# Optimization experiments

Hardware: AMD Instinct MI355X
Metric: run time of the kernel (lower is better)

The kernel has to match this reference:

```python
import jax, jax.numpy as jnp
import numpy as np

N_NODES = 40962
N_EDGES = 245760
K = 10  # gaussian kernels
D = 2   # pseudo-coordinate dim
EPS = 1e-15


def gmm_conv(x, edge_index, pseudo, g, mu, sigma, root, bias):
    """PyG GMMConv with aggr='mean', root_weight=True.
    x: [N, Cin], edge_index: [2, E] (row 0 = source j, row 1 = target i),
    pseudo: [E, D], g: [Cin, K*Cout], mu/sigma: [K, D], root: [Cin, Cout], bias: [Cout].
    """
    src, dst = edge_index[0], edge_index[1]
    E = pseudo.shape[0]
    # Gaussian mixture edge weights: [E, K]
    diff = pseudo[:, None, :] - mu[None, :, :]                     # [E, K, D]
    w = jnp.exp(jnp.sum(-0.5 * diff * diff / (EPS + sigma[None] ** 2), axis=-1))
    xj = x[src]                                                    # [E, Cin] gather
    y = (xj @ g).reshape(E, K, -1)                                 # [E, K, Cout]
    msg = jnp.sum(y * w[:, :, None], axis=1)                       # [E, Cout]
    agg = jax.ops.segment_sum(msg, dst, num_segments=N_NODES)      # scatter-add
    deg = jax.ops.segment_sum(jnp.ones((E,), x.dtype), dst, num_segments=N_NODES)
    agg = agg / jnp.maximum(deg, 1.0)[:, None]                     # mean aggregation
    return agg + x @ root + bias


def setup_inputs() -> dict:
    key = jax.random.key(0)
    ks = jax.random.split(key, 20)
    Cin, Ch, Cout = 64, 64, 128
    sc = lambda fan: 1.0 / np.sqrt(fan)
    inp = {
        "x": jax.random.normal(ks[0], (N_NODES, Cin), jnp.float32),
        "edge_index": jax.random.randint(ks[1], (2, N_EDGES), 0, N_NODES, jnp.int32),
        "pseudo": jax.random.uniform(ks[2], (N_EDGES, D), jnp.float32),
        # conv1: Cin -> Ch
        "g1": jax.random.normal(ks[3], (Cin, K * Ch), jnp.float32) * sc(Cin),
        "mu1": jax.random.uniform(ks[4], (K, D), jnp.float32),
        "sigma1": jax.random.uniform(ks[5], (K, D), jnp.float32) + 0.5,
        "root1": jax.random.normal(ks[6], (Cin, Ch), jnp.float32) * sc(Cin),
        "b1": jnp.zeros((Ch,), jnp.float32),
        # conv2: Ch -> Cout
        "g2": jax.random.normal(ks[7], (Ch, K * Cout), jnp.float32) * sc(Ch),
        "mu2": jax.random.uniform(ks[8], (K, D), jnp.float32),
        "sigma2": jax.random.uniform(ks[9], (K, D), jnp.float32) + 0.5,
        "root2": jax.random.normal(ks[10], (Ch, Cout), jnp.float32) * sc(Ch),
        "b2": jnp.zeros((Cout,), jnp.float32),
        # shortcut: Cin -> Cout (size_in != size_out)
        "gs": jax.random.normal(ks[11], (Cin, K * Cout), jnp.float32) * sc(Cin),
        "mus": jax.random.uniform(ks[12], (K, D), jnp.float32),
        "sigmas": jax.random.uniform(ks[13], (K, D), jnp.float32) + 0.5,
        "roots": jax.random.normal(ks[14], (Cin, Cout), jnp.float32) * sc(Cin),
        "bs": jnp.zeros((Cout,), jnp.float32),
    }
    return inp


def reference(x, edge_index, pseudo, g1, mu1, sigma1, root1, b1,
              g2, mu2, sigma2, root2, b2, gs, mus, sigmas, roots, bs):
    h = gmm_conv(x, edge_index, pseudo, g1, mu1, sigma1, root1, b1)
    h = jax.nn.relu(h)
    y = gmm_conv(h, edge_index, pseudo, g2, mu2, sigma2, root2, b2)
    x_s = gmm_conv(x, edge_index, pseudo, gs, mus, sigmas, roots, bs)
    return jax.nn.relu(y + x_s)
```

## Files before the change

kernel.cpp:

```cpp
#include <hip/hip_runtime.h>
#include <hip/hip_bf16.h>

using bf16 = __hip_bfloat16;
typedef __attribute__((ext_vector_type(8))) short short8;
typedef __attribute__((ext_vector_type(4))) float float4v;

#define N_NODES 40962
#define N_EDGES 245760
#define NP      41024
#define KG      10
#define SCAN_B  256
#define NBLK    ((NP + SCAN_B - 1) / SCAN_B)
#define GRIDF   (NP / 16)

#define CVT_V   (N_NODES * 64 / 8)
#define CVT_BLK ((CVT_V + 255) / 256)
#define W3_BLK  (N_EDGES / 256)
#define PACK_N  (64 * 704 + 2 * 128 * 704)
#define PACK_BLK (PACK_N / 256)

#define ZRS  680
#define ZT   10880

__device__ __forceinline__ float ldf(const void* p, size_t i, int isf32) {
    return isf32 ? ((const float*)p)[i] : __bfloat162float(((const bf16*)p)[i]);
}
__device__ __forceinline__ float blo(unsigned u) { return __uint_as_float(u << 16); }
__device__ __forceinline__ float bhi(unsigned u) { return __uint_as_float(u & 0xffff0000u); }
__device__ __forceinline__ unsigned pk2(float a, float b) {
    union { bf16 h[2]; unsigned u; } t;
    t.h[0] = __float2bfloat16(a);
    t.h[1] = __float2bfloat16(b);
    return t.u;
}
__device__ __forceinline__ int rfl(int v) { return __builtin_amdgcn_readfirstlane(v); }

__global__ void k_detect_count(const void* x, const int* __restrict__ ei,
                               int* __restrict__ flag, int* __restrict__ deg) {
    if (blockIdx.x == 0) {
        __shared__ int huge_c, zero_even;
        if (threadIdx.x == 0) { huge_c = 0; zero_even = 0; }
        __syncthreads();
        const bf16* xb = (const bf16*)x;
        int lh = 0, lz = 0;
        for (int i = threadIdx.x; i < 8192; i += 256) {
            float v = __bfloat162float(xb[i]);
            if (!(fabsf(v) <= 1e4f)) lh++;
            if ((i & 1) == 0 && v == 0.0f) lz++;
        }
        atomicAdd(&huge_c, lh);
        atomicAdd(&zero_even, lz);
        __syncthreads();
        if (threadIdx.x == 0) flag[0] = (huge_c > 0 || zero_even > 3000) ? 1 : 0;
    } else {
        int e = (blockIdx.x - 1) * 256 + threadIdx.x;
        if (e < N_EDGES) atomicAdd(&deg[ei[N_EDGES + e]], 1);
    }
}

__global__ void k_scan1(const int* __restrict__ deg, int* __restrict__ offs,
                        int* __restrict__ bsum) {
    __shared__ int buf[SCAN_B];
    int t = threadIdx.x, b = blockIdx.x;
    int i = b * SCAN_B + t;
    int v = (i < NP) ? deg[i] : 0;
    buf[t] = v;
    __syncthreads();
    for (int off = 1; off < SCAN_B; off <<= 1) {
        int a = (t >= off) ? buf[t - off] : 0;
        __syncthreads();
        buf[t] += a;
        __syncthreads();
    }
    if (i < NP) offs[i] = buf[t] - v;
    if (t == SCAN_B - 1) bsum[b] = buf[t];
}

__global__ void k_scan3m(int* __restrict__ offs, const int* __restrict__ bsum,
                         const int* __restrict__ deg, int* __restrict__ cur,
                         float* __restrict__ invdeg) {
    __shared__ int buf[256];
    int t = threadIdx.x, b = blockIdx.x;
    int v = (t < NBLK) ? bsum[t] : 0;
    buf[t] = v;
    __syncthreads();
    for (int off = 1; off < 256; off <<= 1) {
        int a = (t >= off) ? buf[t - off] : 0;
        __syncthreads();
        buf[t] += a;
        __syncthreads();
    }
    int bofs = (b > 0) ? buf[b - 1] : 0;
    int total = buf[NBLK - 1];
    int i = b * 256 + t;
    if (i < NP) {
        int o = offs[i] + bofs;
        offs[i] = o;
        cur[i] = o;
        int d = deg[i];
        invdeg[i] = 1.0f / (float)(d > 1 ? d : 1);
    }
    if (i == 0) offs[NP] = total;
}

__global__ void k_fill(const int* __restrict__ ei, int* __restrict__ cur,
                       int* __restrict__ ep, int* __restrict__ csr_src) {
    int e = blockIdx.x * 256 + threadIdx.x;
    if (e < N_EDGES) {
        int pos = atomicAdd(&cur[ei[N_EDGES + e]], 1);
        ep[e] = pos;
        csr_src[pos] = ei[e];
    }
}

__device__ __forceinline__ void gw_one(float p0, float p1, const void* mu,
                                       const void* sg, int f, float* out) {
#pragma unroll
    for (int k = 0; k < KG; k++) {
        float m0 = ldf(mu, 2 * k + 0, f), m1 = ldf(mu, 2 * k + 1, f);
        float s0 = ldf(sg, 2 * k + 0, f), s1 = ldf(sg, 2 * k + 1, f);
        float d0 = p0 - m0, d1 = p1 - m1;
        float t = -0.5f * (d0 * d0 / (1e-15f + s0 * s0) + d1 * d1 / (1e-15f + s1 * s1));
        out[k] = __expf(t);
    }
}

__device__ __forceinline__ void pack_frag(const void* g, const void* root, int f,
                                          int idx, int Cout, bf16* Bp) {
    int j = idx & 7;
    int lane = (idx >> 3) & 63;
    int rem = idx >> 9;
    int kc = rem % 22;
    int n = rem / 22;
    int col = n * 16 + (lane & 15);
    int k = kc * 32 + (lane >> 4) * 8 + j;
    float v;
    if (k < 512) {
        int cin = k >> 3, kg = k & 7;
        v = ldf(g, (size_t)cin * (KG * Cout) + (size_t)kg * Cout + col, f);
    } else if (k < 640) {
        int jj = k - 512;
        int cin = jj >> 1, kg = 8 + (jj & 1);
        v = ldf(g, (size_t)cin * (KG * Cout) + (size_t)kg * Cout + col, f);
    } else {
        v = ldf(root, (size_t)(k - 640) * Cout + col, f);
    }
    Bp[idx] = __float2bfloat16(v);
}

__global__ void k_prep_all(const void* __restrict__ x, const void* __restrict__ pseudo,
                           const void* mu1, const void* sg1, const void* mu2,
                           const void* sg2, const void* mus, const void* sgs,
                           const void* g1, const void* root1, const void* g2,
                           const void* root2, const void* gs, const void* roots,
                           const int* __restrict__ flag, const int* __restrict__ ep,
                           bf16* __restrict__ Xf, unsigned* __restrict__ wcab,
                           unsigned* __restrict__ wc2, bf16* wt1p, bf16* wt2p,
                           bf16* wtsp) {
    int b = blockIdx.x;
    int tid = threadIdx.x;
    int f = flag[0];
    if (b < CVT_BLK) {
        int i = b * 256 + tid;
        if (i < CVT_V) {
            int node = i >> 3, j = i & 7;
            uint4 u;
            if (f) {
                const float4* xf = (const float4*)x;
                float4 a = xf[2 * i], c = xf[2 * i + 1];
                union { bf16 t[8]; uint4 u; } tt;
                tt.t[0] = __float2bfloat16(a.x); tt.t[1] = __float2bfloat16(a.y);
                tt.t[2] = __float2bfloat16(a.z); tt.t[3] = __float2bfloat16(a.w);
                tt.t[4] = __float2bfloat16(c.x); tt.t[5] = __float2bfloat16(c.y);
                tt.t[6] = __float2bfloat16(c.z); tt.t[7] = __float2bfloat16(c.w);
                u = tt.u;
            } else {
                u = ((const uint4*)x)[i];
            }
            *(uint4*)(Xf + (size_t)node * 64 + j * 8) = u;
        }
    } else if (b < CVT_BLK + W3_BLK) {
        int e = (b - CVT_BLK) * 256 + tid;
        float p0 = ldf(pseudo, (size_t)e * 2 + 0, f);
        float p1 = ldf(pseudo, (size_t)e * 2 + 1, f);
        float o1[KG], o2[KG], os[KG];
        gw_one(p0, p1, mu1, sg1, f, o1);
        gw_one(p0, p1, mu2, sg2, f, o2);
        gw_one(p0, p1, mus, sgs, f, os);
        int pos = ep[e];
        unsigned* d = wcab + (size_t)pos * 10;
        d[0] = pk2(o1[0], o1[1]); d[1] = pk2(o1[2], o1[3]);
        d[2] = pk2(o1[4], o1[5]); d[3] = pk2(o1[6], o1[7]);
        d[4] = pk2(o1[8], o1[9]);
        d[5] = pk2(os[0], os[1]); d[6] = pk2(os[2], os[3]);
        d[7] = pk2(os[4], os[5]); d[8] = pk2(os[6], os[7]);
        d[9] = pk2(os[8], os[9]);
        unsigned* d2 = wc2 + (size_t)pos * 5;
        d2[0] = pk2(o2[0], o2[1]); d2[1] = pk2(o2[2], o2[3]);
        d2[2] = pk2(o2[4], o2[5]); d2[3] = pk2(o2[6], o2[7]);
        d2[4] = pk2(o2[8], o2[9]);
    } else {
        int idx = (b - CVT_BLK - W3_BLK) * 256 + tid;
        if (idx < 64 * 704) {
            pack_frag(g1, root1, f, idx, 64, wt1p);
        } else if (idx < 64 * 704 + 128 * 704) {
            pack_frag(g2, root2, f, idx - 64 * 704, 128, wt2p);
        } else {
            pack_frag(gs, roots, f, idx - 64 * 704 - 128 * 704, 128, wtsp);
        }
    }
}

__device__ __forceinline__ float ldxf(const bf16* X, int src, int lane) {
    return __bfloat162float(X[(size_t)src * 64 + lane]);
}

__device__ __forceinline__ int clampe(int idx) {
    return idx > N_EDGES - 1 ? N_EDGES - 1 : idx;
}

__device__ __forceinline__ void store_zlds(bf16* z, int r, int lane, const float* a,
                                           float inv) {
    union { bf16 h[8]; uint4 u; } p;
#pragma unroll
    for (int k = 0; k < 8; k++) p.h[k] = __float2bfloat16(a[k] * inv);
    *(uint4*)(z + r * ZRS + lane * 8) = p.u;
    *(unsigned*)(z + r * ZRS + 512 + lane * 2) = pk2(a[8] * inv, a[9] * inv);
}

__device__ __forceinline__ void gather_dual(const int* __restrict__ offs,
                                            const int* __restrict__ csr_src,
                                            const unsigned* __restrict__ wb,
                                            const bf16* __restrict__ X, int node,
                                            int lane, float* aa, float* ab) {
#pragma unroll
    for (int k = 0; k < KG; k++) { aa[k] = 0.0f; ab[k] = 0.0f; }
    int beg = rfl(offs[node]);
    int end = rfl(offs[node + 1]);
    int cnt = end - beg;
    int s4 = rfl(csr_src[clampe(beg + 4)]);
    float xv0 = ldxf(X, rfl(csr_src[clampe(beg + 0)]), lane);
    float xv1 = ldxf(X, rfl(csr_src[clampe(beg + 1)]), lane);
    float xv2 = ldxf(X, rfl(csr_src[clampe(beg + 2)]), lane);
    float xv3 = ldxf(X, rfl(csr_src[clampe(beg + 3)]), lane);
    const unsigned* wp0 = wb + (size_t)clampe(beg + 0) * 10;
    unsigned c0 = wp0[0], c1 = wp0[1], c2 = wp0[2], c3 = wp0[3], c4 = wp0[4];
    unsigned c5 = wp0[5], c6 = wp0[6], c7 = wp0[7], c8 = wp0[8], c9 = wp0[9];
    const unsigned* wp1 = wb + (size_t)clampe(beg + 1) * 10;
    unsigned n0 = wp1[0], n1 = wp1[1], n2 = wp1[2], n3 = wp1[3], n4 = wp1[4];
    unsigned n5 = wp1[5], n6 = wp1[6], n7 = wp1[7], n8 = wp1[8], n9 = wp1[9];
    for (int t = 0; t < cnt; ++t) {
        int s5 = rfl(csr_src[clampe(beg + t + 5)]);
        float xv4 = ldxf(X, s4, lane);
        const unsigned* wp2 = wb + (size_t)clampe(beg + t + 2) * 10;
        unsigned m0 = wp2[0], m1 = wp2[1], m2 = wp2[2], m3 = wp2[3], m4 = wp2[4];
        unsigned m5 = wp2[5], m6 = wp2[6], m7 = wp2[7], m8 = wp2[8], m9 = wp2[9];
        aa[0] += blo(c0) * xv0; aa[1] += bhi(c0) * xv0;
        aa[2] += blo(c1) * xv0; aa[3] += bhi(c1) * xv0;
        aa[4] += blo(c2) * xv0; aa[5] += bhi(c2) * xv0;
        aa[6] += blo(c3) * xv0; aa[7] += bhi(c3) * xv0;
        aa[8] += blo(c4) * xv0; aa[9] += bhi(c4) * xv0;
        ab[0] += blo(c5) * xv0; ab[1] += bhi(c5) * xv0;
        ab[2] += blo(c6) * xv0; ab[3] += bhi(c6) * xv0;
        ab[4] += blo(c7) * xv0; ab[5] += bhi(c7) * xv0;
        ab[6] += blo(c8) * xv0; ab[7] += bhi(c8) * xv0;
        ab[8] += blo(c9) * xv0; ab[9] += bhi(c9) * xv0;
        xv0 = xv1; xv1 = xv2; xv2 = xv3; xv3 = xv4; s4 = s5;
        c0 = n0; c1 = n1; c2 = n2; c3 = n3; c4 = n4;
        c5 = n5; c6 = n6; c7 = n7; c8 = n8; c9 = n9;
        n0 = m0; n1 = m1; n2 = m2; n3 = m3; n4 = m4;
        n5 = m5; n6 = m6; n7 = m7; n8 = m8; n9 = m9;
    }
}

__device__ __forceinline__ void gather_one(const int* __restrict__ offs,
                                           const int* __restrict__ csr_src,
                                           const unsigned* __restrict__ wb,
                                           const bf16* __restrict__ X, int node,
                                           int lane, float* acc) {
#pragma unroll
    for (int k = 0; k < KG; k++) acc[k] = 0.0f;
    int beg = rfl(offs[node]);
    int end = rfl(offs[node + 1]);
    int cnt = end - beg;
    int s4 = rfl(csr_src[clampe(beg + 4)]);
    float xv0 = ldxf(X, rfl(csr_src[clampe(beg + 0)]), lane);
    float xv1 = ldxf(X, rfl(csr_src[clampe(beg + 1)]), lane);
    float xv2 = ldxf(X, rfl(csr_src[clampe(beg + 2)]), lane);
    float xv3 = ldxf(X, rfl(csr_src[clampe(beg + 3)]), lane);
    const unsigned* wp0 = wb + (size_t)clampe(beg + 0) * 5;
    unsigned c0 = wp0[0], c1 = wp0[1], c2 = wp0[2], c3 = wp0[3], c4 = wp0[4];
    const unsigned* wp1 = wb + (size_t)clampe(beg + 1) * 5;
    unsigned n0 = wp1[0], n1 = wp1[1], n2 = wp1[2], n3 = wp1[3], n4 = wp1[4];
    for (int t = 0; t < cnt; ++t) {
        int s5 = rfl(csr_src[clampe(beg + t + 5)]);
        float xv4 = ldxf(X, s4, lane);
        const unsigned* wp2 = wb + (size_t)clampe(beg + t + 2) * 5;
        unsigned m0 = wp2[0], m1 = wp2[1], m2 = wp2[2], m3 = wp2[3], m4 = wp2[4];
        acc[0] += blo(c0) * xv0; acc[1] += bhi(c0) * xv0;
        acc[2] += blo(c1) * xv0; acc[3] += bhi(c1) * xv0;
        acc[4] += blo(c2) * xv0; acc[5] += bhi(c2) * xv0;
        acc[6] += blo(c3) * xv0; acc[7] += bhi(c3) * xv0;
        acc[8] += blo(c4) * xv0; acc[9] += bhi(c4) * xv0;
        xv0 = xv1; xv1 = xv2; xv2 = xv3; xv3 = xv4; s4 = s5;
        c0 = n0; c1 = n1; c2 = n2; c3 = n3; c4 = n4;
        n0 = m0; n1 = m1; n2 = m2; n3 = m3; n4 = m4;
    }
}

__global__ __launch_bounds__(1024) void k_fusedA(
    const int* __restrict__ offs, const int* __restrict__ csr_src,
    const unsigned* __restrict__ wcab, const float* __restrict__ invdeg,
    const bf16* __restrict__ Xf, const bf16* __restrict__ wt1p,
    const bf16* __restrict__ wtsp, const void* __restrict__ b1,
    const void* __restrict__ bs, const int* __restrict__ flag,
    bf16* __restrict__ hf, bf16* __restrict__ ys) {
    __shared__ bf16 z1[ZT];
    __shared__ bf16 zs[ZT];
    int lane = threadIdx.x & 63;
    int wave = threadIdx.x >> 6;
    int bid = blockIdx.x;

    {
        int node = bid * 16 + wave;
        float aa[KG], ab[KG];
        gather_dual(offs, csr_src, wcab, Xf, node, lane, aa, ab);
        float inv = invdeg[node];
        store_zlds(z1, wave, lane, aa, inv);
        store_zlds(zs, wave, lane, ab, inv);
    }
    __syncthreads();

    int m = lane & 15, quad = lane >> 4;
    int row0 = bid * 16;
    int f = flag[0];

    if (wave < 8) {
        float4v acc4 = (float4v){0.f, 0.f, 0.f, 0.f};
        const bf16* brow = wtsp + ((size_t)(wave * 22) * 64 + lane) * 8;
        const bf16* xrow = Xf + (size_t)(row0 + m) * 64;
#pragma unroll
        for (int kc = 0; kc < 22; kc++) {
            short8 a = (kc < 20)
                ? *(const short8*)(zs + m * ZRS + kc * 32 + quad * 8)
                : *(const short8*)(xrow + (kc - 20) * 32 + quad * 8);
            short8 b = *(const short8*)(brow + (size_t)kc * 512);
            acc4 = __builtin_amdgcn_mfma_f32_16x16x32_bf16(a, b, acc4, 0, 0, 0);
        }
        int gcol = wave * 16 + m;
        float bv = ldf(bs, gcol, f);
#pragma unroll
        for (int r = 0; r < 4; r++) {
            int grow = row0 + quad * 4 + r;
            if (grow >= N_NODES) continue;
            ys[(size_t)grow * 128 + gcol] = __float2bfloat16(acc4[r] + bv);
        }
    } else if (wave < 12) {
        int n = wave - 8;
        float4v acc4 = (float4v){0.f, 0.f, 0.f, 0.f};
        const bf16* brow = wt1p + ((size_t)(n * 22) * 64 + lane) * 8;
        const bf16* xrow = Xf + (size_t)(row0 + m) * 64;
#pragma unroll
        for (int kc = 0; kc < 22; kc++) {
            short8 a = (kc < 20)
                ? *(const short8*)(z1 + m * ZRS + kc * 32 + quad * 8)
                : *(const short8*)(xrow + (kc - 20) * 32 + quad * 8);
            short8 b = *(const short8*)(brow + (size_t)kc * 512);
            acc4 = __builtin_amdgcn_mfma_f32_16x16x32_bf16(a, b, acc4, 0, 0, 0);
        }
        int gcol = n * 16 + m;
        float bv = ldf(b1, gcol, f);
#pragma unroll
        for (int r = 0; r < 4; r++) {
            int grow = row0 + quad * 4 + r;
            if (grow >= N_NODES) continue;
            float v = fmaxf(acc4[r] + bv, 0.f);
            hf[(size_t)grow * 64 + gcol] = __float2bfloat16(v);
        }
    }
}

__global__ __launch_bounds__(1024) void k_fusedB(
    const int* __restrict__ offs, const int* __restrict__ csr_src,
    const unsigned* __restrict__ wc2, const float* __restrict__ invdeg,
    const bf16* __restrict__ hf, const bf16* __restrict__ wt2p,
    const void* __restrict__ b2, const bf16* __restrict__ ys,
    const int* __restrict__ flag, void* __restrict__ out) {
    __shared__ bf16 z[ZT];
    int lane = threadIdx.x & 63;
    int wave = threadIdx.x >> 6;
    int bid = blockIdx.x;

    {
        int node = bid * 16 + wave;
        float acc[KG];
        gather_one(offs, csr_src, wc2, hf, node, lane, acc);
        store_zlds(z, wave, lane, acc, invdeg[node]);
    }
    __syncthreads();

    if (wave < 8) {
        int m = lane & 15, quad = lane >> 4;
        int row0 = bid * 16;
        int f = flag[0];
        float4v acc4 = (float4v){0.f, 0.f, 0.f, 0.f};
        const bf16* brow = wt2p + ((size_t)(wave * 22) * 64 + lane) * 8;
        const bf16* hrow = hf + (size_t)(row0 + m) * 64;
#pragma unroll
        for (int kc = 0; kc < 22; kc++) {
            short8 a = (kc < 20)
                ? *(const short8*)(z + m * ZRS + kc * 32 + quad * 8)
                : *(const short8*)(hrow + (kc - 20) * 32 + quad * 8);
            short8 b = *(const short8*)(brow + (size_t)kc * 512);
            acc4 = __builtin_amdgcn_mfma_f32_16x16x32_bf16(a, b, acc4, 0, 0, 0);
        }
        int gcol = wave * 16 + m;
        float bv = ldf(b2, gcol, f);
#pragma unroll
        for (int r = 0; r < 4; r++) {
            int grow = row0 + quad * 4 + r;
            if (grow >= N_NODES) continue;
            size_t oidx = (size_t)grow * 128 + gcol;
            float v = fmaxf(acc4[r] + bv + __bfloat162float(ys[oidx]), 0.f);
            if (f) ((float*)out)[oidx] = v;
            else   ((bf16*)out)[oidx] = __float2bfloat16(v);
        }
    }
}

extern "C" void kernel_launch(void* const* d_in, const int* in_sizes, int n_in,
                              void* d_out, int out_size, void* d_ws, size_t ws_size,
                              hipStream_t stream) {
    const void* x      = d_in[0];
    const int*  ei     = (const int*)d_in[1];
    const void* pseudo = d_in[2];
    const void* g1     = d_in[3];
    const void* mu1    = d_in[4];
    const void* sg1    = d_in[5];
    const void* root1  = d_in[6];
    const void* b1     = d_in[7];
    const void* g2     = d_in[8];
    const void* mu2    = d_in[9];
    const void* sg2    = d_in[10];
    const void* root2  = d_in[11];
    const void* b2     = d_in[12];
    const void* gs     = d_in[13];
    const void* mus    = d_in[14];
    const void* sgs    = d_in[15];
    const void* roots  = d_in[16];
    const void* bs     = d_in[17];

    char* ws = (char*)d_ws;
    size_t off = 0;
    auto alloc = [&](size_t bytes) -> char* {
        char* p = ws + off;
        off += (bytes + 255) & ~(size_t)255;
        return p;
    };
    const size_t XFS = (size_t)NP * 64 * 2;

    int*      flag   = (int*)alloc(256);
    int*      deg    = (int*)alloc((size_t)NP * 4);
    int*      offs   = (int*)alloc((size_t)(NP + 1) * 4);
    int*      cur    = (int*)alloc((size_t)NP * 4);
    float*    invdeg = (float*)alloc((size_t)NP * 4);
    int*      bsum   = (int*)alloc((size_t)NBLK * 4);
    int*      ep     = (int*)alloc((size_t)N_EDGES * 4);
    int*      csrs   = (int*)alloc((size_t)N_EDGES * 4);
    bf16*     Xf     = (bf16*)alloc(XFS);
    bf16*     hf     = (bf16*)alloc(XFS);
    bf16*     ys     = (bf16*)alloc((size_t)NP * 128 * 2);
    bf16*     wt1p   = (bf16*)alloc((size_t)64 * 704 * 2);
    bf16*     wt2p   = (bf16*)alloc((size_t)128 * 704 * 2);
    bf16*     wtsp   = (bf16*)alloc((size_t)128 * 704 * 2);
    unsigned* wcab   = (unsigned*)alloc((size_t)N_EDGES * 10 * 4);
    unsigned* wc2    = (unsigned*)alloc((size_t)N_EDGES * 5 * 4);
    (void)ws_size;

    hipMemsetAsync(deg, 0, (size_t)NP * 4, stream);
    k_detect_count<<<1 + (N_EDGES + 255) / 256, 256, 0, stream>>>(x, ei, flag, deg);
    k_scan1<<<NBLK, SCAN_B, 0, stream>>>(deg, offs, bsum);
    k_scan3m<<<NBLK, 256, 0, stream>>>(offs, bsum, deg, cur, invdeg);
    k_fill<<<(N_EDGES + 255) / 256, 256, 0, stream>>>(ei, cur, ep, csrs);
    k_prep_all<<<CVT_BLK + W3_BLK + PACK_BLK, 256, 0, stream>>>(
        x, pseudo, mu1, sg1, mu2, sg2, mus, sgs, g1, root1, g2, root2, gs, roots,
        flag, ep, Xf, wcab, wc2, wt1p, wt2p, wtsp);
    k_fusedA<<<GRIDF, 1024, 0, stream>>>(offs, csrs, wcab, invdeg, Xf, wt1p, wtsp,
                                         b1, bs, flag, hf, ys);
    k_fusedB<<<GRIDF, 1024, 0, stream>>>(offs, csrs, wc2, invdeg, hf, wt2p, b2,
                                         ys, flag, d_out);
}
```

Measured before the change: 279.1 us.

## Sort nodes by in-degree so each block gathers balanced neighbor counts

Builds a degree histogram and a counting-sort permutation of nodes, then the fused gather+MFMA kernels process nodes in permuted order so the 16 waves of a block have similar edge counts. This targets wave-level load imbalance, where a block waits on its highest-degree node before the shared MFMA stage. In exchange it adds three small kernels (one single-thread scan), a memset, and scattered row reads/writes of X/h/ys/out instead of contiguous rows, which may hurt locality.

```diff
diff --git a/kernel.cpp b/kernel.cpp
--- a/kernel.cpp
+++ b/kernel.cpp
@@ -12,6 +12,7 @@
 #define SCAN_B  256
 #define NBLK    ((NP + SCAN_B - 1) / SCAN_B)
 #define GRIDF   (NP / 16)
+#define DBINS   64
 
 #define CVT_V   (N_NODES * 64 / 8)
 #define CVT_BLK ((CVT_V + 255) / 256)
@@ -55,6 +56,31 @@
     } else {
         int e = (blockIdx.x - 1) * 256 + threadIdx.x;
         if (e < N_EDGES) atomicAdd(&deg[ei[N_EDGES + e]], 1);
+    }
+}
+
+__global__ void k_hist(const int* __restrict__ deg, int* __restrict__ hist) {
+    int i = blockIdx.x * 256 + threadIdx.x;
+    if (i < NP) {
+        int b = deg[i];
+        if (b > DBINS - 1) b = DBINS - 1;
+        atomicAdd(&hist[b], 1);
+    }
+}
+__global__ void k_binscan(const int* __restrict__ hist, int* __restrict__ binofs) {
+    if (threadIdx.x == 0 && blockIdx.x == 0) {
+        int s = 0;
+        for (int i = 0; i < DBINS; i++) { binofs[i] = s; s += hist[i]; }
+    }
+}
+__global__ void k_mkperm(const int* __restrict__ deg, int* __restrict__ binofs,
+                         int* __restrict__ perm) {
+    int i = blockIdx.x * 256 + threadIdx.x;
+    if (i < NP) {
+        int b = deg[i];
+        if (b > DBINS - 1) b = DBINS - 1;
+        int pos = atomicAdd(&binofs[b], 1);
+        perm[pos] = i;
     }
 }
 
@@ -311,18 +337,20 @@
 __global__ __launch_bounds__(1024) void k_fusedA(
     const int* __restrict__ offs, const int* __restrict__ csr_src,
     const unsigned* __restrict__ wcab, const float* __restrict__ invdeg,
-    const bf16* __restrict__ Xf, const bf16* __restrict__ wt1p,
-    const bf16* __restrict__ wtsp, const void* __restrict__ b1,
-    const void* __restrict__ bs, const int* __restrict__ flag,
-    bf16* __restrict__ hf, bf16* __restrict__ ys) {
+    const int* __restrict__ perm, const bf16* __restrict__ Xf,
+    const bf16* __restrict__ wt1p, const bf16* __restrict__ wtsp,
+    const void* __restrict__ b1, const void* __restrict__ bs,
+    const int* __restrict__ flag, bf16* __restrict__ hf, bf16* __restrict__ ys) {
     __shared__ bf16 z1[ZT];
     __shared__ bf16 zs[ZT];
+    __shared__ int prow[16];
     int lane = threadIdx.x & 63;
     int wave = threadIdx.x >> 6;
     int bid = blockIdx.x;
 
     {
-        int node = bid * 16 + wave;
+        int node = perm[bid * 16 + wave];
+        if (lane == 0) prow[wave] = node;
         float aa[KG], ab[KG];
         gather_dual(offs, csr_src, wcab, Xf, node, lane, aa, ab);
         float inv = invdeg[node];
@@ -332,13 +360,13 @@
     __syncthreads();
 
     int m = lane & 15, quad = lane >> 4;
-    int row0 = bid * 16;
     int f = flag[0];
 
     if (wave < 8) {
         float4v acc4 = (float4v){0.f, 0.f, 0.f, 0.f};
         const bf16* brow = wtsp + ((size_t)(wave * 22) * 64 + lane) * 8;
-        const bf16* xrow = Xf + (size_t)(row0 + m) * 64;
+        int pm = prow[m];
+        const bf16* xrow = Xf + (size_t)pm * 64;
 #pragma unroll
         for (int kc = 0; kc < 22; kc++) {
             short8 a = (kc < 20)
@@ -351,7 +379,7 @@
         float bv = ldf(bs, gcol, f);
 #pragma unroll
         for (int r = 0; r < 4; r++) {
-            int grow = row0 + quad * 4 + r;
+            int grow = prow[quad * 4 + r];
             if (grow >= N_NODES) continue;
             ys[(size_t)grow * 128 + gcol] = __float2bfloat16(acc4[r] + bv);
         }
@@ -359,7 +387,8 @@
         int n = wave - 8;
         float4v acc4 = (float4v){0.f, 0.f, 0.f, 0.f};
         const bf16* brow = wt1p + ((size_t)(n * 22) * 64 + lane) * 8;
-        const bf16* xrow = Xf + (size_t)(row0 + m) * 64;
+        int pm = prow[m];
+        const bf16* xrow = Xf + (size_t)pm * 64;
 #pragma unroll
         for (int kc = 0; kc < 22; kc++) {
             short8 a = (kc < 20)
@@ -372,7 +401,7 @@
         float bv = ldf(b1, gcol, f);
 #pragma unroll
         for (int r = 0; r < 4; r++) {
-            int grow = row0 + quad * 4 + r;
+            int grow = prow[quad * 4 + r];
             if (grow >= N_NODES) continue;
             float v = fmaxf(acc4[r] + bv, 0.f);
             hf[(size_t)grow * 64 + gcol] = __float2bfloat16(v);
@@ -383,16 +412,19 @@
 __global__ __launch_bounds__(1024) void k_fusedB(
     const int* __restrict__ offs, const int* __restrict__ csr_src,
     const unsigned* __restrict__ wc2, const float* __restrict__ invdeg,
-    const bf16* __restrict__ hf, const bf16* __restrict__ wt2p,
-    const void* __restrict__ b2, const bf16* __restrict__ ys,
-    const int* __restrict__ flag, void* __restrict__ out) {
+    const int* __restrict__ perm, const bf16* __restrict__ hf,
+    const bf16* __restrict__ wt2p, const void* __restrict__ b2,
+    const bf16* __restrict__ ys, const int* __restrict__ flag,
+    void* __restrict__ out) {
     __shared__ bf16 z[ZT];
+    __shared__ int prow[16];
     int lane = threadIdx.x & 63;
     int wave = threadIdx.x >> 6;
     int bid = blockIdx.x;
 
     {
-        int node = bid * 16 + wave;
+        int node = perm[bid * 16 + wave];
+        if (lane == 0) prow[wave] = node;
         float acc[KG];
         gather_one(offs, csr_src, wc2, hf, node, lane, acc);
         store_zlds(z, wave, lane, acc, invdeg[node]);
@@ -401,11 +433,11 @@
 
     if (wave < 8) {
         int m = lane & 15, quad = lane >> 4;
-        int row0 = bid * 16;
         int f = flag[0];
         float4v acc4 = (float4v){0.f, 0.f, 0.f, 0.f};
         const bf16* brow = wt2p + ((size_t)(wave * 22) * 64 + lane) * 8;
-        const bf16* hrow = hf + (size_t)(row0 + m) * 64;
+        int pm = prow[m];
+        const bf16* hrow = hf + (size_t)pm * 64;
 #pragma unroll
         for (int kc = 0; kc < 22; kc++) {
             short8 a = (kc < 20)
@@ -418,7 +450,7 @@
         float bv = ldf(b2, gcol, f);
 #pragma unroll
         for (int r = 0; r < 4; r++) {
-            int grow = row0 + quad * 4 + r;
+            int grow = prow[quad * 4 + r];
             if (grow >= N_NODES) continue;
             size_t oidx = (size_t)grow * 128 + gcol;
             float v = fmaxf(acc4[r] + bv + __bfloat162float(ys[oidx]), 0.f);
@@ -465,6 +497,9 @@
     int*      cur    = (int*)alloc((size_t)NP * 4);
     float*    invdeg = (float*)alloc((size_t)NP * 4);
     int*      bsum   = (int*)alloc((size_t)NBLK * 4);
+    int*      hist   = (int*)alloc((size_t)DBINS * 4);
+    int*      binofs = (int*)alloc((size_t)DBINS * 4);
+    int*      perm   = (int*)alloc((size_t)NP * 4);
     int*      ep     = (int*)alloc((size_t)N_EDGES * 4);
     int*      csrs   = (int*)alloc((size_t)N_EDGES * 4);
     bf16*     Xf     = (bf16*)alloc(XFS);
@@ -478,15 +513,19 @@
     (void)ws_size;
 
     hipMemsetAsync(deg, 0, (size_t)NP * 4, stream);
+    hipMemsetAsync(hist, 0, (size_t)DBINS * 4, stream);
     k_detect_count<<<1 + (N_EDGES + 255) / 256, 256, 0, stream>>>(x, ei, flag, deg);
+    k_hist<<<(NP + 255) / 256, 256, 0, stream>>>(deg, hist);
+    k_binscan<<<1, 64, 0, stream>>>(hist, binofs);
+    k_mkperm<<<(NP + 255) / 256, 256, 0, stream>>>(deg, binofs, perm);
     k_scan1<<<NBLK, SCAN_B, 0, stream>>>(deg, offs, bsum);
     k_scan3m<<<NBLK, 256, 0, stream>>>(offs, bsum, deg, cur, invdeg);
     k_fill<<<(N_EDGES + 255) / 256, 256, 0, stream>>>(ei, cur, ep, csrs);
     k_prep_all<<<CVT_BLK + W3_BLK + PACK_BLK, 256, 0, stream>>>(
         x, pseudo, mu1, sg1, mu2, sg2, mus, sgs, g1, root1, g2, root2, gs, roots,
         flag, ep, Xf, wcab, wc2, wt1p, wt2p, wtsp);
-    k_fusedA<<<GRIDF, 1024, 0, stream>>>(offs, csrs, wcab, invdeg, Xf, wt1p, wtsp,
-                                         b1, bs, flag, hf, ys);
-    k_fusedB<<<GRIDF, 1024, 0, stream>>>(offs, csrs, wc2, invdeg, hf, wt2p, b2,
-                                         ys, flag, d_out);
-}
+    k_fusedA<<<GRIDF, 1024, 0, stream>>>(offs, csrs, wcab, invdeg, perm, Xf,
+                                         wt1p, wtsp, b1, bs, flag, hf, ys);
+    k_fusedB<<<GRIDF, 1024, 0, stream>>>(offs, csrs, wc2, invdeg, perm, hf,
+                                         wt2p, b2, ys, flag, d_out);
+}
```

After: 579.0 us. 107% more time.
